# Optimization experiments

Hardware: AMD Instinct MI355X
Metric: run time of the kernel (lower is better)

## Reference

```python
import jax, jax.numpy as jnp
import numpy as np

N_NODES = 50000
N_EDGES = 800000
F_IN, F_HID, F_OUT = 1433, 64, 32


def setup_inputs() -> dict:
    key = jax.random.key(0)
    ks = jax.random.split(key, 8)
    x = jax.random.normal(ks[0], (N_NODES, F_IN), dtype=jnp.float32)
    edge_index = jax.random.randint(ks[1], (2, N_EDGES), 0, N_NODES, dtype=jnp.int32)
    s1 = 1.0 / np.sqrt(F_IN)
    s2 = 1.0 / np.sqrt(F_HID)
    W1_l = jax.random.normal(ks[2], (F_IN, F_HID), dtype=jnp.float32) * s1
    W1_r = jax.random.normal(ks[3], (F_IN, F_HID), dtype=jnp.float32) * s1
    b1 = jnp.zeros((F_HID,), dtype=jnp.float32)
    W2_l = jax.random.normal(ks[4], (F_HID, F_OUT), dtype=jnp.float32) * s2
    W2_r = jax.random.normal(ks[5], (F_HID, F_OUT), dtype=jnp.float32) * s2
    b2 = jnp.zeros((F_OUT,), dtype=jnp.float32)
    return {"x": x, "edge_index": edge_index, "W1_l": W1_l, "b1": b1,
            "W1_r": W1_r, "W2_l": W2_l, "b2": b2, "W2_r": W2_r}


def sage_conv(x, src, dst, W_l, b_l, W_r, num_nodes):
    # PyG SAGEConv: out = lin_l(mean_{j in N(i)} x_j) + lin_r(x_i)
    # lin_l is linear, so project first then aggregate (saves E x F_in gather).
    msg = x @ W_l                                   # [N, F_out]
    agg = jax.ops.segment_sum(msg[src], dst, num_segments=num_nodes)  # [N, F_out]
    deg = jax.ops.segment_sum(jnp.ones_like(src, dtype=x.dtype), dst,
                              num_segments=num_nodes)                 # [N]
    agg = jnp.where(deg[:, None] > 0, agg / jnp.maximum(deg, 1.0)[:, None], 0.0)
    return agg + b_l + x @ W_r


def reference(x, edge_index, W1_l, b1, W1_r, W2_l, b2, W2_r):
    src, dst = edge_index[0], edge_index[1]
    n = x.shape[0]
    h = sage_conv(x, src, dst, W1_l, b1, W1_r, n)   # [N, 64]  (no activation between convs)
    h = sage_conv(h, src, dst, W2_l, b2, W2_r, n)   # [N, 32]
    h = jax.nn.relu(h)
    # dropout p=0.5 is identity in eval mode
    return jax.nn.log_softmax(h, axis=1)
```

## Files before the change

kernel.cpp:

```cpp
#include <hip/hip_runtime.h>
#include <hip/hip_bf16.h>
#include <cstdint>
#include <cstddef>


#define N_NODES 50000
#define N_EDGES 800000
#define F_IN    1433
#define KP      1472
#define NCH     6
#define DMAX    64
#define NBLK_GEMM 1563
#define NBLK_FILL 3125

typedef __attribute__((ext_vector_type(8))) short bf16x8;
typedef __attribute__((ext_vector_type(4))) float f32x4;

static constexpr size_t OFF_H1PRE = 0;
static constexpr size_t OFF_M2    = OFF_H1PRE + 25600000;
static constexpr size_t OFF_CUR   = OFF_M2    + 12800000;
static constexpr size_t OFF_ESRC  = OFF_CUR   + 200000;
static constexpr size_t OFF_WT    = OFF_ESRC  + 12800000;

__device__ inline ushort f2bf(float f) {
  union { float f; uint32_t u; } v; v.f = f;
  uint32_t u = v.u + 0x7FFFu + ((v.u >> 16) & 1u);
  return (ushort)(u >> 16);
}

__device__ __forceinline__ void gload_lds16(const void* g, void* l) {
  __builtin_amdgcn_global_load_lds(
      (const __attribute__((address_space(1))) void*)g,
      (__attribute__((address_space(3))) void*)l, 16, 0, 0);
}

__global__ __launch_bounds__(256) void k_init(const float* __restrict__ Wl,
                                              const float* __restrict__ Wr,
                                              ushort* __restrict__ Wt,
                                              int* __restrict__ cur) {
  const int bid = blockIdx.x;
  if (bid < 768) {
    const int c  = bid & 127;
    const int k  = (bid >> 7) * 256 + threadIdx.x;
    if (k >= KP) return;
    float v = 0.f;
    if (k < F_IN) v = (c < 64) ? Wl[k * 64 + c] : Wr[k * 64 + (c - 64)];
    Wt[(size_t)c * KP + k] = f2bf(v);
  } else {
    int i = (bid - 768) * 256 + threadIdx.x;
    if (i < N_NODES) cur[i] = 0;
  }
}

__global__ __launch_bounds__(256) void k_gemm1cf(const float* __restrict__ x,
                                                 const ushort* __restrict__ Wt,
                                                 float* __restrict__ h1pre,
                                                 const int* __restrict__ ei,
                                                 int* __restrict__ cur,
                                                 int* __restrict__ esrc) {
  if (blockIdx.x >= NBLK_GEMM) {
    int e = (blockIdx.x - NBLK_GEMM) * 256 + threadIdx.x;
    if (e < N_EDGES) {
      int s = ei[e];
      int d = ei[N_EDGES + e];
      int slot = atomicAdd(&cur[d], 1);
      if (slot < DMAX) esrc[(size_t)d * DMAX + slot] = s;
    }
    return;
  }

  __shared__ __align__(16) ushort As[4][32 * 64];
  __shared__ __align__(16) ushort Bs[4][128 * 64];
  const int t    = threadIdx.x;
  const int lane = t & 63;
  const int w    = t >> 6;
  const int wr   = w >> 1;
  const int wc   = w & 1;
  const int row0 = blockIdx.x * 32;

  const int ar = t >> 3;
  const int aq = t & 7;
  const size_t abase = (size_t)(row0 + ar) * F_IN + aq * 8;
  const size_t LIM   = (size_t)N_NODES * F_IN - 4;
  const int aoff = ar * 64;
  const int asw  = (aq ^ (ar & 7)) * 8;

  const int lr = lane >> 3, lt = lane & 7;
  const ushort* b_src[4];
  ushort* b_dst[4];
#pragma unroll
  for (int j = 0; j < 4; ++j) {
    int r = (w * 4 + j) * 8 + lr;
    b_src[j] = Wt + (size_t)r * KP + (lt ^ (r & 7)) * 8;
    b_dst[j] = (ushort*)&Bs[0][(w * 4 + j) * 512];
  }

  f32x4 acc[4] = {};
  f32x4 av[4][2];

#define LOADA_CHUNK(kbase)                                          \
  do {                                                              \
    _Pragma("unroll")                                               \
    for (int s = 0; s < 4; ++s) {                                   \
      size_t i0 = abase + (size_t)(kbase) + s * 64;                 \
      size_t i1 = i0 + 4;                                           \
      if (i0 > LIM) i0 = LIM;                                       \
      if (i1 > LIM) i1 = LIM;                                       \
      __builtin_memcpy(&av[s][0], x + i0, 16);                      \
      __builtin_memcpy(&av[s][1], x + i1, 16);                      \
    }                                                               \
  } while (0)

  LOADA_CHUNK(0);

  for (int c = 0; c < NCH; ++c) {
    const int kbase = c * 256;
    const int nsub = (c < 5) ? 4 : 3;
#pragma unroll
    for (int s = 0; s < 4; ++s) {
      if (s < nsub) {
        bf16x8 w0;
#pragma unroll
        for (int e = 0; e < 4; ++e) {
          w0[e]     = (short)f2bf(av[s][0][e]);
          w0[4 + e] = (short)f2bf(av[s][1][e]);
        }
        *(bf16x8*)&As[s][aoff + asw] = w0;
      }
    }
#pragma unroll
    for (int s = 0; s < 4; ++s) {
      if (s < nsub) {
#pragma unroll
        for (int j = 0; j < 4; ++j)
          gload_lds16(b_src[j] + kbase + s * 64, b_dst[j] + (size_t)s * (128 * 64));
      }
    }
    __syncthreads();
    if (c + 1 < NCH) LOADA_CHUNK(kbase + 256);
    const int nks = (c < 5) ? 8 : 6;
#pragma unroll
    for (int kk = 0; kk < 8; ++kk) {
      if (kk < nks) {
        const int sub = kk >> 1;
        const int sbase = (kk & 1) * 4 + (lane >> 4);
        bf16x8 a, b[4];
        {
          int r = wr * 16 + (lane & 15);
          int s2 = sbase ^ (r & 7);
          a = *(const bf16x8*)&As[sub][r * 64 + s2 * 8];
        }
#pragma unroll
        for (int n = 0; n < 4; ++n) {
          int r = wc * 64 + n * 16 + (lane & 15);
          int s2 = sbase ^ (r & 7);
          b[n] = *(const bf16x8*)&Bs[sub][r * 64 + s2 * 8];
        }
#pragma unroll
        for (int n = 0; n < 4; ++n)
          acc[n] = __builtin_amdgcn_mfma_f32_16x16x32_bf16(a, b[n], acc[n], 0, 0, 0);
      }
    }
    __syncthreads();
  }
#undef LOADA_CHUNK

  {
    int rbase = row0 + wr * 16 + (lane >> 4) * 4;
#pragma unroll
    for (int n = 0; n < 4; ++n) {
      int col = wc * 64 + n * 16 + (lane & 15);
#pragma unroll
      for (int r = 0; r < 4; ++r) {
        int grow = rbase + r;
        if (grow < N_NODES) h1pre[(size_t)grow * 128 + col] = acc[n][r];
      }
    }
  }
}

__global__ __launch_bounds__(256) void k_agg1mm(const float* __restrict__ h1pre,
                                                const int* __restrict__ cur,
                                                const int* __restrict__ esrc,
                                                const float* __restrict__ b1,
                                                const float* __restrict__ W2l,
                                                const float* __restrict__ W2r,
                                                float* __restrict__ m2) {
  __shared__ __align__(16) ushort Hs[32][72];
  __shared__ __align__(16) ushort Ws[64][72];
  const int t = threadIdx.x;
  const int lane = t & 63;
  const int w = t >> 6;

#pragma unroll
  for (int i = 0; i < 16; ++i) {
    int idx = t + 256 * i;
    int k = idx >> 6, c = idx & 63;
    float v = (c < 32) ? W2l[k * 32 + c] : W2r[k * 32 + (c - 32)];
    Ws[c][k] = f2bf(v);
  }

  const float bl = b1[lane];
  const int dbase = blockIdx.x * 32 + w * 8;
#pragma unroll 1
  for (int i = 0; i < 8; ++i) {
    const int d = dbase + i;
    ushort hv = 0;
    if (d < N_NODES) {
      int dg = cur[d]; if (dg > DMAX) dg = DMAX;
      const size_t base = (size_t)d * DMAX;
      float a0 = 0.f, a1 = 0.f, a2 = 0.f, a3 = 0.f;
      float a4 = 0.f, a5 = 0.f, a6 = 0.f, a7 = 0.f;
      int j = 0;
      for (; j + 8 <= dg; j += 8) {
        int s0 = esrc[base + j],     s1 = esrc[base + j + 1];
        int s2 = esrc[base + j + 2], s3 = esrc[base + j + 3];
        int s4 = esrc[base + j + 4], s5 = esrc[base + j + 5];
        int s6 = esrc[base + j + 6], s7 = esrc[base + j + 7];
        a0 += h1pre[(size_t)s0 * 128 + lane];
        a1 += h1pre[(size_t)s1 * 128 + lane];
        a2 += h1pre[(size_t)s2 * 128 + lane];
        a3 += h1pre[(size_t)s3 * 128 + lane];
        a4 += h1pre[(size_t)s4 * 128 + lane];
        a5 += h1pre[(size_t)s5 * 128 + lane];
        a6 += h1pre[(size_t)s6 * 128 + lane];
        a7 += h1pre[(size_t)s7 * 128 + lane];
      }
      for (; j + 4 <= dg; j += 4) {
        int s0 = esrc[base + j],     s1 = esrc[base + j + 1];
        int s2 = esrc[base + j + 2], s3 = esrc[base + j + 3];
        a0 += h1pre[(size_t)s0 * 128 + lane];
        a1 += h1pre[(size_t)s1 * 128 + lane];
        a2 += h1pre[(size_t)s2 * 128 + lane];
        a3 += h1pre[(size_t)s3 * 128 + lane];
      }
      for (; j < dg; ++j) a0 += h1pre[(size_t)esrc[base + j] * 128 + lane];
      float acc = ((a0 + a1) + (a2 + a3)) + ((a4 + a5) + (a6 + a7));
      const float inv = (dg > 0) ? 1.f / (float)dg : 0.f;
      float h = acc * inv + bl + h1pre[(size_t)d * 128 + 64 + lane];
      hv = f2bf(h);
    }
    Hs[w * 8 + i][lane] = hv;
  }
  __syncthreads();

  const int wr2 = w >> 1;
  f32x4 acc2[2] = {};
#pragma unroll
  for (int j = 0; j < 2; ++j) {
    bf16x8 a;
    {
      int r = wr2 * 16 + (lane & 15);
      a = *(const bf16x8*)&Hs[r][j * 32 + (lane >> 4) * 8];
    }
#pragma unroll
    for (int n = 0; n < 2; ++n) {
      int c = ((w & 1) * 2 + n) * 16 + (lane & 15);
      bf16x8 b = *(const bf16x8*)&Ws[c][j * 32 + (lane >> 4) * 8];
      acc2[n] = __builtin_amdgcn_mfma_f32_16x16x32_bf16(a, b, acc2[n], 0, 0, 0);
    }
  }
  {
    int rbase = blockIdx.x * 32 + wr2 * 16 + (lane >> 4) * 4;
#pragma unroll
    for (int n = 0; n < 2; ++n) {
      int col = ((w & 1) * 2 + n) * 16 + (lane & 15);
#pragma unroll
      for (int r = 0; r < 4; ++r) {
        int grow = rbase + r;
        if (grow < N_NODES) m2[(size_t)grow * 64 + col] = acc2[n][r];
      }
    }
  }
}

__global__ __launch_bounds__(256) void k_agg2(const float* __restrict__ m2,
                                              const int* __restrict__ cur,
                                              const int* __restrict__ esrc,
                                              const float* __restrict__ b2,
                                              float* __restrict__ out) {
  const int lane = threadIdx.x & 63;
  const int half = lane >> 5;
  const int f = lane & 31;
  const int d = blockIdx.x * 8 + ((threadIdx.x >> 6) << 1) + half;
  int dg = cur[d]; if (dg > DMAX) dg = DMAX;
  const size_t base = (size_t)d * DMAX;
  float a0 = 0.f, a1 = 0.f, a2 = 0.f, a3 = 0.f;
  float a4 = 0.f, a5 = 0.f, a6 = 0.f, a7 = 0.f;
  int j = 0;
  for (; j + 8 <= dg; j += 8) {
    int s0 = esrc[base + j],     s1 = esrc[base + j + 1];
    int s2 = esrc[base + j + 2], s3 = esrc[base + j + 3];
    int s4 = esrc[base + j + 4], s5 = esrc[base + j + 5];
    int s6 = esrc[base + j + 6], s7 = esrc[base + j + 7];
    a0 += m2[(size_t)s0 * 64 + f];
    a1 += m2[(size_t)s1 * 64 + f];
    a2 += m2[(size_t)s2 * 64 + f];
    a3 += m2[(size_t)s3 * 64 + f];
    a4 += m2[(size_t)s4 * 64 + f];
    a5 += m2[(size_t)s5 * 64 + f];
    a6 += m2[(size_t)s6 * 64 + f];
    a7 += m2[(size_t)s7 * 64 + f];
  }
  for (; j + 4 <= dg; j += 4) {
    int s0 = esrc[base + j],     s1 = esrc[base + j + 1];
    int s2 = esrc[base + j + 2], s3 = esrc[base + j + 3];
    a0 += m2[(size_t)s0 * 64 + f];
    a1 += m2[(size_t)s1 * 64 + f];
    a2 += m2[(size_t)s2 * 64 + f];
    a3 += m2[(size_t)s3 * 64 + f];
  }
  for (; j < dg; ++j) a0 += m2[(size_t)esrc[base + j] * 64 + f];
  float acc = ((a0 + a1) + (a2 + a3)) + ((a4 + a5) + (a6 + a7));
  const float inv = (dg > 0) ? 1.f / (float)dg : 0.f;
  float v = acc * inv + b2[f] + m2[(size_t)d * 64 + 32 + f];
  v = fmaxf(v, 0.f);
  float m = v;
#pragma unroll
  for (int o = 16; o > 0; o >>= 1) m = fmaxf(m, __shfl_xor(m, o, 32));
  float e = expf(v - m);
  float sum = e;
#pragma unroll
  for (int o = 16; o > 0; o >>= 1) sum += __shfl_xor(sum, o, 32);
  out[(size_t)d * 32 + f] = v - m - logf(sum);
}

extern "C" void kernel_launch(void* const* d_in, const int* in_sizes, int n_in,
                              void* d_out, int out_size, void* d_ws, size_t ws_size,
                              hipStream_t stream) {
  const float* x   = (const float*)d_in[0];
  const int*   ei  = (const int*)d_in[1];
  const float* W1l = (const float*)d_in[2];
  const float* b1  = (const float*)d_in[3];
  const float* W1r = (const float*)d_in[4];
  const float* W2l = (const float*)d_in[5];
  const float* b2  = (const float*)d_in[6];
  const float* W2r = (const float*)d_in[7];
  float* out = (float*)d_out;

  char* ws = (char*)d_ws;
  float*  h1pre = (float*)(ws + OFF_H1PRE);
  float*  m2    = (float*)(ws + OFF_M2);
  int*    cur   = (int*)(ws + OFF_CUR);
  int*    esrc  = (int*)(ws + OFF_ESRC);
  ushort* Wt    = (ushort*)(ws + OFF_WT);

  k_init<<<768 + (N_NODES + 255) / 256, 256, 0, stream>>>(W1l, W1r, Wt, cur);

  k_gemm1cf<<<NBLK_GEMM + NBLK_FILL, 256, 0, stream>>>(x, Wt, h1pre, ei, cur, esrc);

  k_agg1mm<<<(N_NODES + 31) / 32, 256, 0, stream>>>(h1pre, cur, esrc, b1,
                                                    W2l, W2r, m2);
  k_agg2<<<N_NODES / 8, 256, 0, stream>>>(m2, cur, esrc, b2, out);
}
```

Baseline: 184.5 us.

## Pre-tile weights into MFMA fragment layout and load B directly from global

The bf16 weight matrix is now stored pre-permuted into 16-column by 8-k fragments that match the MFMA B operand layout. Each lane then loads its B fragment straight from global memory (L2/L1 cached) instead of staging the whole 128x256 B tile through LDS via global_load_lds. This removes 64KB of LDS per block, which could raise occupancy, and drops the B-staging traffic. In exchange, every wave re-reads weights from the cache hierarchy on each k-step, adding global-load latency inside the MFMA loop.

```diff
diff --git a/kernel.cpp b/kernel.cpp
--- a/kernel.cpp
+++ b/kernel.cpp
@@ -8,6 +8,7 @@
 #define N_EDGES 800000
 #define F_IN    1433
 #define KP      1472
+#define NKB     184
 #define NCH     6
 #define DMAX    64
 #define NBLK_GEMM 1563
@@ -28,15 +29,9 @@
   return (ushort)(u >> 16);
 }
 
-__device__ __forceinline__ void gload_lds16(const void* g, void* l) {
-  __builtin_amdgcn_global_load_lds(
-      (const __attribute__((address_space(1))) void*)g,
-      (__attribute__((address_space(3))) void*)l, 16, 0, 0);
-}
-
 __global__ __launch_bounds__(256) void k_init(const float* __restrict__ Wl,
                                               const float* __restrict__ Wr,
-                                              ushort* __restrict__ Wt,
+                                              ushort* __restrict__ Wt2,
                                               int* __restrict__ cur) {
   const int bid = blockIdx.x;
   if (bid < 768) {
@@ -45,7 +40,8 @@
     if (k >= KP) return;
     float v = 0.f;
     if (k < F_IN) v = (c < 64) ? Wl[k * 64 + c] : Wr[k * 64 + (c - 64)];
-    Wt[(size_t)c * KP + k] = f2bf(v);
+    size_t idx = (((size_t)(c >> 4) * NKB + (k >> 3)) * 16 + (c & 15)) * 8 + (k & 7);
+    Wt2[idx] = f2bf(v);
   } else {
     int i = (bid - 768) * 256 + threadIdx.x;
     if (i < N_NODES) cur[i] = 0;
@@ -53,7 +49,7 @@
 }
 
 __global__ __launch_bounds__(256) void k_gemm1cf(const float* __restrict__ x,
-                                                 const ushort* __restrict__ Wt,
+                                                 const ushort* __restrict__ Wt2,
                                                  float* __restrict__ h1pre,
                                                  const int* __restrict__ ei,
                                                  int* __restrict__ cur,
@@ -70,7 +66,6 @@
   }
 
   __shared__ __align__(16) ushort As[4][32 * 64];
-  __shared__ __align__(16) ushort Bs[4][128 * 64];
   const int t    = threadIdx.x;
   const int lane = t & 63;
   const int w    = t >> 6;
@@ -85,15 +80,7 @@
   const int aoff = ar * 64;
   const int asw  = (aq ^ (ar & 7)) * 8;
 
-  const int lr = lane >> 3, lt = lane & 7;
-  const ushort* b_src[4];
-  ushort* b_dst[4];
-#pragma unroll
-  for (int j = 0; j < 4; ++j) {
-    int r = (w * 4 + j) * 8 + lr;
-    b_src[j] = Wt + (size_t)r * KP + (lt ^ (r & 7)) * 8;
-    b_dst[j] = (ushort*)&Bs[0][(w * 4 + j) * 512];
-  }
+  const ushort* bbase = Wt2 + (size_t)(lane & 15) * 8;
 
   f32x4 acc[4] = {};
   f32x4 av[4][2];
@@ -128,14 +115,6 @@
         *(bf16x8*)&As[s][aoff + asw] = w0;
       }
     }
-#pragma unroll
-    for (int s = 0; s < 4; ++s) {
-      if (s < nsub) {
-#pragma unroll
-        for (int j = 0; j < 4; ++j)
-          gload_lds16(b_src[j] + kbase + s * 64, b_dst[j] + (size_t)s * (128 * 64));
-      }
-    }
     __syncthreads();
     if (c + 1 < NCH) LOADA_CHUNK(kbase + 256);
     const int nks = (c < 5) ? 8 : 6;
@@ -150,11 +129,11 @@
           int s2 = sbase ^ (r & 7);
           a = *(const bf16x8*)&As[sub][r * 64 + s2 * 8];
         }
+        const int kb = (kbase >> 3) + kk * 4 + (lane >> 4);
 #pragma unroll
         for (int n = 0; n < 4; ++n) {
-          int r = wc * 64 + n * 16 + (lane & 15);
-          int s2 = sbase ^ (r & 7);
-          b[n] = *(const bf16x8*)&Bs[sub][r * 64 + s2 * 8];
+          int ct = wc * 4 + n;
+          __builtin_memcpy(&b[n], bbase + ((size_t)ct * NKB + kb) * 128, 16);
         }
 #pragma unroll
         for (int n = 0; n < 4; ++n)
@@ -343,11 +322,11 @@
   float*  m2    = (float*)(ws + OFF_M2);
   int*    cur   = (int*)(ws + OFF_CUR);
   int*    esrc  = (int*)(ws + OFF_ESRC);
-  ushort* Wt    = (ushort*)(ws + OFF_WT);
-
-  k_init<<<768 + (N_NODES + 255) / 256, 256, 0, stream>>>(W1l, W1r, Wt, cur);
-
-  k_gemm1cf<<<NBLK_GEMM + NBLK_FILL, 256, 0, stream>>>(x, Wt, h1pre, ei, cur, esrc);
+  ushort* Wt2   = (ushort*)(ws + OFF_WT);
+
+  k_init<<<768 + (N_NODES + 255) / 256, 256, 0, stream>>>(W1l, W1r, Wt2, cur);
+
+  k_gemm1cf<<<NBLK_GEMM + NBLK_FILL, 256, 0, stream>>>(x, Wt2, h1pre, ei, cur, esrc);
 
   k_agg1mm<<<(N_NODES + 31) / 32, 256, 0, stream>>>(h1pre, cur, esrc, b1,
                                                     W2l, W2r, m2);
```

New measurement: 190.2 us. 1.03x slower.
